# Performance work log

Measured on AMD Instinct MI355X. Metric: run time of the kernel, lower is better.

Reference implementation:

```python
import jax, jax.numpy as jnp
import numpy as np

B, M, QT, KVT, H = 2, 16, 1024, 4096, 128


def setup_inputs() -> dict:
    key = jax.random.key(0)
    kq, kk = jax.random.split(key)
    q = jax.random.normal(kq, (B, M, QT, H), dtype=jnp.float32)
    k = jax.random.normal(kk, (B, M, KVT, H), dtype=jnp.float32)
    return {"q": q, "k": k}


def reference(q, k):
    # Original: broadcast multiply q[B,M,QT,1,H] * k[B,M,1,KVT,H], sum over H.
    # Mathematically identical to a batched QK^T contraction over head dim.
    # score: [B, M, QT, KVT]
    return jnp.einsum('bmqh,bmkh->bmqk', q, k)
```

## Files before the change

### kernel.cpp

```cpp
#include <hip/hip_runtime.h>


#define QT   1024
#define KVT  4096
#define HD   128
#define NBM  32
#define NXCD 8

using bf16x8 = __attribute__((ext_vector_type(8))) __bf16;
using bf16x4 = __attribute__((ext_vector_type(4))) __bf16;
using f32x4  = __attribute__((ext_vector_type(4))) float;

__global__ __launch_bounds__(256, 2)
void QKBmm_74062416052397_kernel(const float* __restrict__ q,
                                 const float* __restrict__ k,
                                 float* __restrict__ out) {
    __shared__ __bf16 As[128 * 128];
    __shared__ __bf16 Bs[128 * 128];

    const int t = threadIdx.x;

    const unsigned lin = blockIdx.x;
    const unsigned swz = (lin & (NXCD - 1)) * (8192u / NXCD) + (lin >> 3);
    const int nt_ = swz & 31;
    const int mt  = (swz >> 5) & 7;
    const int bm  = swz >> 8;
    const int m0  = mt * 128;
    const int n0  = nt_ * 128;

    const float* __restrict__ Qp = q + ((size_t)bm * QT  + m0) * HD;
    const float* __restrict__ Kp = k + ((size_t)bm * KVT + n0) * HD;

#pragma unroll
    for (int i = 0; i < 16; ++i) {
        int f   = i * 256 + t;
        int row = f >> 5;
        float4 va = reinterpret_cast<const float4*>(Qp)[f];
        float4 vb = reinterpret_cast<const float4*>(Kp)[f];
        bf16x4 pa = { (__bf16)va.x, (__bf16)va.y, (__bf16)va.z, (__bf16)va.w };
        bf16x4 pb = { (__bf16)vb.x, (__bf16)vb.y, (__bf16)vb.z, (__bf16)vb.w };
        int e = (f << 2) ^ ((row & 7) << 3);
        *reinterpret_cast<bf16x4*>(&As[e]) = pa;
        *reinterpret_cast<bf16x4*>(&Bs[e]) = pb;
    }
    __syncthreads();

    const int lane = t & 63;
    const int wid  = t >> 6;
    const int wm   = (wid >> 1) * 64;
    const int wn   = (wid & 1) * 64;
    const int lr   = lane & 15;
    const int lg   = lane >> 4;

    f32x4 acc[4][4] = {};

#pragma unroll
    for (int ks = 0; ks < 4; ++ks) {
        const int kcol = ks * 32 + lg * 8;
        bf16x8 af[4], bfr[4];
#pragma unroll
        for (int mi = 0; mi < 4; ++mi) {
            int r = wm + mi * 16 + lr;
            int e = (r * 128 + kcol) ^ ((r & 7) << 3);
            af[mi] = *reinterpret_cast<const bf16x8*>(&As[e]);
        }
#pragma unroll
        for (int ni = 0; ni < 4; ++ni) {
            int r = wn + ni * 16 + lr;
            int e = (r * 128 + kcol) ^ ((r & 7) << 3);
            bfr[ni] = *reinterpret_cast<const bf16x8*>(&Bs[e]);
        }
#pragma unroll
        for (int mi = 0; mi < 4; ++mi)
#pragma unroll
            for (int ni = 0; ni < 4; ++ni)
                acc[mi][ni] = __builtin_amdgcn_mfma_f32_16x16x32_bf16(
                    af[mi], bfr[ni], acc[mi][ni], 0, 0, 0);
    }

    float* __restrict__ Cp = out + (size_t)bm * QT * KVT;
#pragma unroll
    for (int mi = 0; mi < 4; ++mi) {
#pragma unroll
        for (int j = 0; j < 4; ++j) {
            int row = m0 + wm + mi * 16 + lg * 4 + j;
            float* rp = Cp + (size_t)row * KVT + n0 + wn;
#pragma unroll
            for (int ni = 0; ni < 4; ++ni)
                __builtin_nontemporal_store(acc[mi][ni][j], rp + ni * 16 + lr);
        }
    }
}

extern "C" void kernel_launch(void* const* d_in, const int* in_sizes, int n_in,
                              void* d_out, int out_size, void* d_ws, size_t ws_size,
                              hipStream_t stream) {
    const float* q = (const float*)d_in[0];
    const float* k = (const float*)d_in[1];
    float* out = (float*)d_out;

    QKBmm_74062416052397_kernel<<<dim3(8192), dim3(256), 0, stream>>>(q, k, out);
}
```

Baseline: 136.3 us.

## Drop LDS staging and load MFMA fragments directly from global memory

Removes the shared-memory tiles and the block barrier. Each wave now loads its Q and K fragments straight from global memory as float4 pairs and converts them to bf16 in registers before the MFMAs. Occupancy is raised from 2 to 3 blocks per CU in launch bounds. Because the two wave-pairs share rows, this re-reads overlapping Q/K data from global or L2 (each element about twice), and the strided per-lane loads are less coalesced than the old staged loads.

```diff
diff --git a/kernel.cpp b/kernel.cpp
--- a/kernel.cpp
+++ b/kernel.cpp
@@ -4,20 +4,15 @@
 #define QT   1024
 #define KVT  4096
 #define HD   128
-#define NBM  32
 #define NXCD 8
 
 using bf16x8 = __attribute__((ext_vector_type(8))) __bf16;
-using bf16x4 = __attribute__((ext_vector_type(4))) __bf16;
 using f32x4  = __attribute__((ext_vector_type(4))) float;
 
-__global__ __launch_bounds__(256, 2)
+__global__ __launch_bounds__(256, 3)
 void QKBmm_74062416052397_kernel(const float* __restrict__ q,
                                  const float* __restrict__ k,
                                  float* __restrict__ out) {
-    __shared__ __bf16 As[128 * 128];
-    __shared__ __bf16 Bs[128 * 128];
-
     const int t = threadIdx.x;
 
     const unsigned lin = blockIdx.x;
@@ -28,23 +23,6 @@
     const int m0  = mt * 128;
     const int n0  = nt_ * 128;
 
-    const float* __restrict__ Qp = q + ((size_t)bm * QT  + m0) * HD;
-    const float* __restrict__ Kp = k + ((size_t)bm * KVT + n0) * HD;
-
-#pragma unroll
-    for (int i = 0; i < 16; ++i) {
-        int f   = i * 256 + t;
-        int row = f >> 5;
-        float4 va = reinterpret_cast<const float4*>(Qp)[f];
-        float4 vb = reinterpret_cast<const float4*>(Kp)[f];
-        bf16x4 pa = { (__bf16)va.x, (__bf16)va.y, (__bf16)va.z, (__bf16)va.w };
-        bf16x4 pb = { (__bf16)vb.x, (__bf16)vb.y, (__bf16)vb.z, (__bf16)vb.w };
-        int e = (f << 2) ^ ((row & 7) << 3);
-        *reinterpret_cast<bf16x4*>(&As[e]) = pa;
-        *reinterpret_cast<bf16x4*>(&Bs[e]) = pb;
-    }
-    __syncthreads();
-
     const int lane = t & 63;
     const int wid  = t >> 6;
     const int wm   = (wid >> 1) * 64;
@@ -52,30 +30,35 @@
     const int lr   = lane & 15;
     const int lg   = lane >> 4;
 
+    const float* __restrict__ Qb = q + ((size_t)bm * QT  + m0 + wm + lr) * HD;
+    const float* __restrict__ Kb = k + ((size_t)bm * KVT + n0 + wn + lr) * HD;
+
     f32x4 acc[4][4] = {};
 
 #pragma unroll
     for (int ks = 0; ks < 4; ++ks) {
-        const int kcol = ks * 32 + lg * 8;
-        bf16x8 af[4], bfr[4];
+        const int kc = ks * 32 + lg * 8;
+        bf16x8 bfr[4];
+#pragma unroll
+        for (int ni = 0; ni < 4; ++ni) {
+            const float* p = Kb + ni * 16 * HD + kc;
+            float4 u0 = *reinterpret_cast<const float4*>(p);
+            float4 u1 = *reinterpret_cast<const float4*>(p + 4);
+            bfr[ni] = bf16x8{ (__bf16)u0.x, (__bf16)u0.y, (__bf16)u0.z, (__bf16)u0.w,
+                              (__bf16)u1.x, (__bf16)u1.y, (__bf16)u1.z, (__bf16)u1.w };
+        }
 #pragma unroll
         for (int mi = 0; mi < 4; ++mi) {
-            int r = wm + mi * 16 + lr;
-            int e = (r * 128 + kcol) ^ ((r & 7) << 3);
-            af[mi] = *reinterpret_cast<const bf16x8*>(&As[e]);
-        }
-#pragma unroll
-        for (int ni = 0; ni < 4; ++ni) {
-            int r = wn + ni * 16 + lr;
-            int e = (r * 128 + kcol) ^ ((r & 7) << 3);
-            bfr[ni] = *reinterpret_cast<const bf16x8*>(&Bs[e]);
-        }
-#pragma unroll
-        for (int mi = 0; mi < 4; ++mi)
+            const float* p = Qb + mi * 16 * HD + kc;
+            float4 u0 = *reinterpret_cast<const float4*>(p);
+            float4 u1 = *reinterpret_cast<const float4*>(p + 4);
+            bf16x8 af = { (__bf16)u0.x, (__bf16)u0.y, (__bf16)u0.z, (__bf16)u0.w,
+                          (__bf16)u1.x, (__bf16)u1.y, (__bf16)u1.z, (__bf16)u1.w };
 #pragma unroll
             for (int ni = 0; ni < 4; ++ni)
                 acc[mi][ni] = __builtin_amdgcn_mfma_f32_16x16x32_bf16(
-                    af[mi], bfr[ni], acc[mi][ni], 0, 0, 0);
+                    af, bfr[ni], acc[mi][ni], 0, 0, 0);
+        }
     }
 
     float* __restrict__ Cp = out + (size_t)bm * QT * KVT;
```

Measured after the change: 273.1 us. +100.4%, slower.

## Split head-dim load into two halves to overlap second load with MFMA

Applied to the files above, without the earlier changes.

The K=128 head dimension is split into two 64-wide halves with separate LDS buffers. The second half's global loads are issued before the first half's MFMAs, so they can overlap with compute, and the second half is converted and stored to LDS afterward. This aims to hide global load latency in a kernel that loads everything once, at the cost of more live registers (32 float4 in flight) that could hurt occupancy at launch_bounds(256,2).

```diff
diff --git a/kernel.cpp b/kernel.cpp
--- a/kernel.cpp
+++ b/kernel.cpp
@@ -4,7 +4,6 @@
 #define QT   1024
 #define KVT  4096
 #define HD   128
-#define NBM  32
 #define NXCD 8
 
 using bf16x8 = __attribute__((ext_vector_type(8))) __bf16;
@@ -15,8 +14,8 @@
 void QKBmm_74062416052397_kernel(const float* __restrict__ q,
                                  const float* __restrict__ k,
                                  float* __restrict__ out) {
-    __shared__ __bf16 As[128 * 128];
-    __shared__ __bf16 Bs[128 * 128];
+    __shared__ __bf16 As[2][128 * 64];
+    __shared__ __bf16 Bs[2][128 * 64];
 
     const int t = threadIdx.x;
 
@@ -28,20 +27,28 @@
     const int m0  = mt * 128;
     const int n0  = nt_ * 128;
 
-    const float* __restrict__ Qp = q + ((size_t)bm * QT  + m0) * HD;
-    const float* __restrict__ Kp = k + ((size_t)bm * KVT + n0) * HD;
+    const float4* __restrict__ Q4 =
+        reinterpret_cast<const float4*>(q + ((size_t)bm * QT  + m0) * HD);
+    const float4* __restrict__ K4 =
+        reinterpret_cast<const float4*>(k + ((size_t)bm * KVT + n0) * HD);
 
+
+    float4 qa[8], ka[8];
 #pragma unroll
-    for (int i = 0; i < 16; ++i) {
-        int f   = i * 256 + t;
-        int row = f >> 5;
-        float4 va = reinterpret_cast<const float4*>(Qp)[f];
-        float4 vb = reinterpret_cast<const float4*>(Kp)[f];
-        bf16x4 pa = { (__bf16)va.x, (__bf16)va.y, (__bf16)va.z, (__bf16)va.w };
-        bf16x4 pb = { (__bf16)vb.x, (__bf16)vb.y, (__bf16)vb.z, (__bf16)vb.w };
-        int e = (f << 2) ^ ((row & 7) << 3);
-        *reinterpret_cast<bf16x4*>(&As[e]) = pa;
-        *reinterpret_cast<bf16x4*>(&Bs[e]) = pb;
+    for (int it = 0; it < 8; ++it) {
+        int f = it * 256 + t, row = f >> 4, c4 = f & 15;
+        qa[it] = Q4[row * 32 + c4];
+        ka[it] = K4[row * 32 + c4];
+    }
+#pragma unroll
+    for (int it = 0; it < 8; ++it) {
+        int f = it * 256 + t, row = f >> 4, c4 = f & 15;
+        int e = (row * 64 + c4 * 4) ^ ((row & 7) << 3);
+        float4 va = qa[it], vb = ka[it];
+        *reinterpret_cast<bf16x4*>(&As[0][e]) =
+            bf16x4{ (__bf16)va.x, (__bf16)va.y, (__bf16)va.z, (__bf16)va.w };
+        *reinterpret_cast<bf16x4*>(&Bs[0][e]) =
+            bf16x4{ (__bf16)vb.x, (__bf16)vb.y, (__bf16)vb.z, (__bf16)vb.w };
     }
     __syncthreads();
 
@@ -54,21 +61,65 @@
 
     f32x4 acc[4][4] = {};
 
+    float4 qb[8], kb[8];
 #pragma unroll
-    for (int ks = 0; ks < 4; ++ks) {
+    for (int it = 0; it < 8; ++it) {
+        int f = it * 256 + t, row = f >> 4, c4 = f & 15;
+        qb[it] = Q4[row * 32 + 16 + c4];
+        kb[it] = K4[row * 32 + 16 + c4];
+    }
+
+#pragma unroll
+    for (int ks = 0; ks < 2; ++ks) {
         const int kcol = ks * 32 + lg * 8;
         bf16x8 af[4], bfr[4];
 #pragma unroll
         for (int mi = 0; mi < 4; ++mi) {
             int r = wm + mi * 16 + lr;
-            int e = (r * 128 + kcol) ^ ((r & 7) << 3);
-            af[mi] = *reinterpret_cast<const bf16x8*>(&As[e]);
+            int e = (r * 64 + kcol) ^ ((r & 7) << 3);
+            af[mi] = *reinterpret_cast<const bf16x8*>(&As[0][e]);
         }
 #pragma unroll
         for (int ni = 0; ni < 4; ++ni) {
             int r = wn + ni * 16 + lr;
-            int e = (r * 128 + kcol) ^ ((r & 7) << 3);
-            bfr[ni] = *reinterpret_cast<const bf16x8*>(&Bs[e]);
+            int e = (r * 64 + kcol) ^ ((r & 7) << 3);
+            bfr[ni] = *reinterpret_cast<const bf16x8*>(&Bs[0][e]);
+        }
+#pragma unroll
+        for (int mi = 0; mi < 4; ++mi)
+#pragma unroll
+            for (int ni = 0; ni < 4; ++ni)
+                acc[mi][ni] = __builtin_amdgcn_mfma_f32_16x16x32_bf16(
+                    af[mi], bfr[ni], acc[mi][ni], 0, 0, 0);
+    }
+
+#pragma unroll
+    for (int it = 0; it < 8; ++it) {
+        int f = it * 256 + t, row = f >> 4, c4 = f & 15;
+        int e = (row * 64 + c4 * 4) ^ ((row & 7) << 3);
+        float4 va = qb[it], vb = kb[it];
+        *reinterpret_cast<bf16x4*>(&As[1][e]) =
+            bf16x4{ (__bf16)va.x, (__bf16)va.y, (__bf16)va.z, (__bf16)va.w };
+        *reinterpret_cast<bf16x4*>(&Bs[1][e]) =
+            bf16x4{ (__bf16)vb.x, (__bf16)vb.y, (__bf16)vb.z, (__bf16)vb.w };
+    }
+    __syncthreads();
+
+#pragma unroll
+    for (int ks = 0; ks < 2; ++ks) {
+        const int kcol = ks * 32 + lg * 8;
+        bf16x8 af[4], bfr[4];
+#pragma unroll
+        for (int mi = 0; mi < 4; ++mi) {
+            int r = wm + mi * 16 + lr;
+            int e = (r * 64 + kcol) ^ ((r & 7) << 3);
+            af[mi] = *reinterpret_cast<const bf16x8*>(&As[1][e]);
+        }
+#pragma unroll
+        for (int ni = 0; ni < 4; ++ni) {
+            int r = wn + ni * 16 + lr;
+            int e = (r * 64 + kcol) ^ ((r & 7) << 3);
+            bfr[ni] = *reinterpret_cast<const bf16x8*>(&Bs[1][e]);
         }
 #pragma unroll
         for (int mi = 0; mi < 4; ++mi)
```

Result: no change. 134.7 us (-1.2%).

## Split head dim into two LDS halves to raise occupancy to four blocks

Applied to the files above, without the earlier changes.

The kernel now stages the 128-wide head dimension in two 64-column halves, which halves shared memory per block (64KB to 32KB). The launch bound rises from 2 to 4 blocks per CU. Loads are issued in two batches of four float4 per half to cap register pressure. The aim is more resident waves to hide global-load latency and overlap the output-store-bound epilogue, at the cost of an extra barrier pair and tighter per-thread register limits.

```diff
diff --git a/kernel.cpp b/kernel.cpp
--- a/kernel.cpp
+++ b/kernel.cpp
@@ -4,19 +4,18 @@
 #define QT   1024
 #define KVT  4096
 #define HD   128
-#define NBM  32
 #define NXCD 8
 
 using bf16x8 = __attribute__((ext_vector_type(8))) __bf16;
 using bf16x4 = __attribute__((ext_vector_type(4))) __bf16;
 using f32x4  = __attribute__((ext_vector_type(4))) float;
 
-__global__ __launch_bounds__(256, 2)
+__global__ __launch_bounds__(256, 4)
 void QKBmm_74062416052397_kernel(const float* __restrict__ q,
                                  const float* __restrict__ k,
                                  float* __restrict__ out) {
-    __shared__ __bf16 As[128 * 128];
-    __shared__ __bf16 Bs[128 * 128];
+    __shared__ __bf16 As[128 * 64];
+    __shared__ __bf16 Bs[128 * 64];
 
     const int t = threadIdx.x;
 
@@ -28,22 +27,10 @@
     const int m0  = mt * 128;
     const int n0  = nt_ * 128;
 
-    const float* __restrict__ Qp = q + ((size_t)bm * QT  + m0) * HD;
-    const float* __restrict__ Kp = k + ((size_t)bm * KVT + n0) * HD;
-
-#pragma unroll
-    for (int i = 0; i < 16; ++i) {
-        int f   = i * 256 + t;
-        int row = f >> 5;
-        float4 va = reinterpret_cast<const float4*>(Qp)[f];
-        float4 vb = reinterpret_cast<const float4*>(Kp)[f];
-        bf16x4 pa = { (__bf16)va.x, (__bf16)va.y, (__bf16)va.z, (__bf16)va.w };
-        bf16x4 pb = { (__bf16)vb.x, (__bf16)vb.y, (__bf16)vb.z, (__bf16)vb.w };
-        int e = (f << 2) ^ ((row & 7) << 3);
-        *reinterpret_cast<bf16x4*>(&As[e]) = pa;
-        *reinterpret_cast<bf16x4*>(&Bs[e]) = pb;
-    }
-    __syncthreads();
+    const float4* __restrict__ Q4 =
+        reinterpret_cast<const float4*>(q + ((size_t)bm * QT  + m0) * HD);
+    const float4* __restrict__ K4 =
+        reinterpret_cast<const float4*>(k + ((size_t)bm * KVT + n0) * HD);
 
     const int lane = t & 63;
     const int wid  = t >> 6;
@@ -55,27 +42,65 @@
     f32x4 acc[4][4] = {};
 
 #pragma unroll
-    for (int ks = 0; ks < 4; ++ks) {
-        const int kcol = ks * 32 + lg * 8;
-        bf16x8 af[4], bfr[4];
+    for (int h = 0; h < 2; ++h) {
+        if (h) __syncthreads();
+
+        float4 qv[4], kv[4];
 #pragma unroll
-        for (int mi = 0; mi < 4; ++mi) {
-            int r = wm + mi * 16 + lr;
-            int e = (r * 128 + kcol) ^ ((r & 7) << 3);
-            af[mi] = *reinterpret_cast<const bf16x8*>(&As[e]);
+        for (int it = 0; it < 4; ++it) {
+            int f = it * 256 + t, row = f >> 4, c4 = f & 15;
+            qv[it] = Q4[row * 32 + h * 16 + c4];
+            kv[it] = K4[row * 32 + h * 16 + c4];
         }
 #pragma unroll
-        for (int ni = 0; ni < 4; ++ni) {
-            int r = wn + ni * 16 + lr;
-            int e = (r * 128 + kcol) ^ ((r & 7) << 3);
-            bfr[ni] = *reinterpret_cast<const bf16x8*>(&Bs[e]);
+        for (int it = 0; it < 4; ++it) {
+            int f = it * 256 + t, row = f >> 4, c4 = f & 15;
+            int e = (row * 64 + c4 * 4) ^ ((row & 7) << 3);
+            *reinterpret_cast<bf16x4*>(&As[e]) =
+                bf16x4{ (__bf16)qv[it].x, (__bf16)qv[it].y, (__bf16)qv[it].z, (__bf16)qv[it].w };
+            *reinterpret_cast<bf16x4*>(&Bs[e]) =
+                bf16x4{ (__bf16)kv[it].x, (__bf16)kv[it].y, (__bf16)kv[it].z, (__bf16)kv[it].w };
         }
 #pragma unroll
-        for (int mi = 0; mi < 4; ++mi)
+        for (int it = 4; it < 8; ++it) {
+            int f = it * 256 + t, row = f >> 4, c4 = f & 15;
+            qv[it - 4] = Q4[row * 32 + h * 16 + c4];
+            kv[it - 4] = K4[row * 32 + h * 16 + c4];
+        }
 #pragma unroll
-            for (int ni = 0; ni < 4; ++ni)
-                acc[mi][ni] = __builtin_amdgcn_mfma_f32_16x16x32_bf16(
-                    af[mi], bfr[ni], acc[mi][ni], 0, 0, 0);
+        for (int it = 4; it < 8; ++it) {
+            int f = it * 256 + t, row = f >> 4, c4 = f & 15;
+            int e = (row * 64 + c4 * 4) ^ ((row & 7) << 3);
+            *reinterpret_cast<bf16x4*>(&As[e]) =
+                bf16x4{ (__bf16)qv[it-4].x, (__bf16)qv[it-4].y, (__bf16)qv[it-4].z, (__bf16)qv[it-4].w };
+            *reinterpret_cast<bf16x4*>(&Bs[e]) =
+                bf16x4{ (__bf16)kv[it-4].x, (__bf16)kv[it-4].y, (__bf16)kv[it-4].z, (__bf16)kv[it-4].w };
+        }
+        __syncthreads();
+
+#pragma unroll
+        for (int ks = 0; ks < 2; ++ks) {
+            const int kcol = ks * 32 + lg * 8;
+            bf16x8 af[4], bfr[4];
+#pragma unroll
+            for (int mi = 0; mi < 4; ++mi) {
+                int r = wm + mi * 16 + lr;
+                int e = (r * 64 + kcol) ^ ((r & 7) << 3);
+                af[mi] = *reinterpret_cast<const bf16x8*>(&As[e]);
+            }
+#pragma unroll
+            for (int ni = 0; ni < 4; ++ni) {
+                int r = wn + ni * 16 + lr;
+                int e = (r * 64 + kcol) ^ ((r & 7) << 3);
+                bfr[ni] = *reinterpret_cast<const bf16x8*>(&Bs[e]);
+            }
+#pragma unroll
+            for (int mi = 0; mi < 4; ++mi)
+#pragma unroll
+                for (int ni = 0; ni < 4; ++ni)
+                    acc[mi][ni] = __builtin_amdgcn_mfma_f32_16x16x32_bf16(
+                        af[mi], bfr[ni], acc[mi][ni], 0, 0, 0);
+        }
     }
 
     float* __restrict__ Cp = out + (size_t)bm * QT * KVT;
```

New measurement: 122.6 us. 10.1% less time.
